# Optimization experiments

Hardware: AMD Instinct MI355X
Metric: run time of the kernel (lower is better)

## Reference

```python
import jax, jax.numpy as jnp
import numpy as np

# Matcher thresholds from detectron2 RPN defaults
IOU_LO, IOU_HI = 0.3, 0.7            # anchor_matcher
OBJ_LO, OBJ_HI = 0.1, 0.3            # objectness_anchor_matcher (lower thresholds)
EPS = 1e-12


def _pairwise_iou(gt, anc):
    # gt: [G,4], anc: [A,4] (x1,y1,x2,y2) -> [G,A]
    area_g = (gt[:, 2] - gt[:, 0]) * (gt[:, 3] - gt[:, 1])
    area_a = (anc[:, 2] - anc[:, 0]) * (anc[:, 3] - anc[:, 1])
    lt = jnp.maximum(gt[:, None, :2], anc[None, :, :2])
    rb = jnp.minimum(gt[:, None, 2:], anc[None, :, 2:])
    wh = jnp.clip(rb - lt, 0.0)
    inter = wh[..., 0] * wh[..., 1]
    union = area_g[:, None] + area_a[None, :] - inter
    return jnp.where(inter > 0, inter / union, 0.0)


def _match(iou, lo, hi):
    # detectron2 Matcher with labels [0,-1,1] and allow_low_quality_matches=True
    vals = iou.max(axis=0)                      # [A]
    idxs = jnp.argmax(iou, axis=0)              # [A]
    labels = jnp.where(vals >= hi, 1, jnp.where(vals >= lo, -1, 0)).astype(jnp.int32)
    highest_per_gt = iou.max(axis=1)            # [G]
    low_quality = (iou == highest_per_gt[:, None]).any(axis=0)  # [A]
    labels = jnp.where(low_quality, 1, labels)
    return idxs, labels


def _get_deltas_linear(anc, tgt):
    # Box2BoxTransformLinear(normalize_by_size=True).get_deltas
    cx = 0.5 * (anc[:, 0] + anc[:, 2])
    cy = 0.5 * (anc[:, 1] + anc[:, 3])
    w = anc[:, 2] - anc[:, 0]
    h = anc[:, 3] - anc[:, 1]
    # order (l, t, r, b)
    deltas = jnp.stack([cx - tgt[:, 0], cy - tgt[:, 1], tgt[:, 2] - cx, tgt[:, 3] - cy], axis=-1)
    return deltas / jnp.stack([w, h, w, h], axis=-1)


def _label_one_image(gt_i, anchors):
    iou = _pairwise_iou(gt_i, anchors)                     # [G,A]
    m_idx, gt_labels = _match(iou, IOU_LO, IOU_HI)
    o_idx, obj_labels = _match(iou, OBJ_LO, OBJ_HI)
    matched_gt_boxes = gt_i[m_idx]                         # [A,4]
    # deltas reordered [:, [0,2,1,3]] -> (left, right, top, bottom)
    d = _get_deltas_linear(anchors, gt_i[o_idx])[:, jnp.array([0, 2, 1, 3])]
    in_box = (d >= 0).all(axis=-1)
    d = jnp.where(in_box[:, None], d, 0.0)
    lr, tb = d[:, 0:2], d[:, 2:4]
    prod = (lr.min(-1) / (lr.max(-1) + EPS)) * (tb.min(-1) / (tb.max(-1) + EPS))
    centerness = jnp.where(prod > 0, jnp.sqrt(jnp.where(prod > 0, prod, 1.0)), 0.0)
    centerness = jnp.where(obj_labels == 0, 0.0, centerness)
    return gt_labels, matched_gt_boxes, obj_labels, centerness


def setup_inputs() -> dict:
    key = jax.random.key(0)
    k1, k2, k3, k4 = jax.random.split(key, 4)
    A, B, G = 200000, 8, 32
    img_wh = jnp.array([1333.0, 800.0], dtype=jnp.float32)
    # anchors: random centers, sizes in [8, 264]
    a_ctr = jax.random.uniform(k1, (A, 2), dtype=jnp.float32) * img_wh
    a_wh = jax.random.uniform(k2, (A, 2), dtype=jnp.float32) * 256.0 + 8.0
    anchors = jnp.concatenate([a_ctr - 0.5 * a_wh, a_ctr + 0.5 * a_wh], axis=-1)
    # gt boxes: [B,G,4], sizes in [16, 416]
    g_ctr = jax.random.uniform(k3, (B, G, 2), dtype=jnp.float32) * img_wh
    g_wh = jax.random.uniform(k4, (B, G, 2), dtype=jnp.float32) * 400.0 + 16.0
    gt_boxes = jnp.concatenate([g_ctr - 0.5 * g_wh, g_ctr + 0.5 * g_wh], axis=-1)
    return {"gt_boxes": gt_boxes, "anchors": anchors}


def reference(gt_boxes, anchors):
    # gt_boxes: [B,G,4]; anchors: [A,4]
    gt_labels, matched_gt_boxes, obj_labels, centerness = jax.vmap(
        lambda g: _label_one_image(g, anchors)
    )(gt_boxes)
    return gt_labels, matched_gt_boxes, obj_labels, centerness
```

## Files before the change

kernel.cpp:

```cpp
#include <hip/hip_runtime.h>

#define G 32
#define APT 4
#define CHUNK (256 * APT)

__device__ __forceinline__ float iou_pre(float sum_area,
                                         float g0, float g1, float g2, float g3,
                                         float a0, float a1, float a2, float a3) {
#pragma clang fp contract(off)
    float ltx = fmaxf(g0, a0), lty = fmaxf(g1, a1);
    float rbx = fminf(g2, a2), rby = fminf(g3, a3);
    float wx = fmaxf(rbx - ltx, 0.0f), wy = fmaxf(rby - lty, 0.0f);
    float inter = wx * wy;
    float uni = sum_area - inter;
    return inter * __builtin_amdgcn_rcpf(uni);
}

__device__ __forceinline__ float centerness_fn(float4 an, float4 tb) {
#pragma clang fp contract(off)
    float cx = 0.5f * (an.x + an.z), cy = 0.5f * (an.y + an.w);
    float w = an.z - an.x, h = an.w - an.y;
    float d0 = (cx - tb.x) / w;
    float d1 = (tb.z - cx) / w;
    float d2 = (cy - tb.y) / h;
    float d3 = (tb.w - cy) / h;
    bool inb = (d0 >= 0.0f) && (d1 >= 0.0f) && (d2 >= 0.0f) && (d3 >= 0.0f);
    if (!inb) { d0 = d1 = d2 = d3 = 0.0f; }
    float prod = (fminf(d0, d1) / (fmaxf(d0, d1) + 1e-12f)) *
                 (fminf(d2, d3) / (fmaxf(d2, d3) + 1e-12f));
    return prod > 0.0f ? sqrtf(prod) : 0.0f;
}

__global__ __launch_bounds__(256) void k1_main(const float* __restrict__ gt,
                                               const float* __restrict__ anchors,
                                               float* __restrict__ out,
                                               float* __restrict__ blockmax,
                                               int A, int B) {
#pragma clang fp contract(off)
    __shared__ float4 s_gt[G];
    __shared__ float s_red[G * 4];
    const int c = blockIdx.x, b = blockIdx.y, t = threadIdx.x;
    if (t < G) s_gt[t] = ((const float4*)gt)[b * G + t];

    const float4* __restrict__ gt4 = (const float4*)gt;

    float4 an[APT];
    float aa[APT], best[APT];
    int bidx[APT];
    bool valid[APT];
    const int abase = c * CHUNK + t;
#pragma unroll
    for (int k = 0; k < APT; ++k) {
        int a = abase + k * 256;
        valid[k] = (a < A);
        int ac = valid[k] ? a : (A - 1);
        an[k] = ((const float4*)anchors)[ac];
        aa[k] = (an[k].z - an[k].x) * (an[k].w - an[k].y);
        best[k] = -1.0f;
        bidx[k] = 0;
    }

    const int lane = t & 63, wid = t >> 6;

#pragma unroll 8
    for (int g = 0; g < G; ++g) {
        const float4 gb = gt4[b * G + g];
        const float ag = (gb.z - gb.x) * (gb.w - gb.y);
        float v[APT];
#pragma unroll
        for (int k = 0; k < APT; ++k) {
            v[k] = iou_pre(ag + aa[k], gb.x, gb.y, gb.z, gb.w,
                           an[k].x, an[k].y, an[k].z, an[k].w);
            if (v[k] > best[k]) { best[k] = v[k]; bidx[k] = g; }
        }
        float lm = fmaxf(fmaxf(v[0], v[1]), fmaxf(v[2], v[3]));
#pragma unroll
        for (int off = 32; off > 0; off >>= 1) lm = fmaxf(lm, __shfl_down(lm, off, 64));
        if (lane == 0) s_red[g * 4 + wid] = lm;
    }
    __syncthreads();
    if (t < G) {
        float v = fmaxf(fmaxf(s_red[t * 4 + 0], s_red[t * 4 + 1]),
                        fmaxf(s_red[t * 4 + 2], s_red[t * 4 + 3]));
        blockmax[(c * B + b) * G + t] = v;
    }

    const size_t BA = (size_t)B * (size_t)A;
    const size_t bA = (size_t)b * (size_t)A;
#pragma unroll
    for (int k = 0; k < APT; ++k) {
        if (!valid[k]) continue;
        const size_t o = bA + (size_t)(abase + k * 256);
        int gl = (best[k] >= 0.7f) ? 1 : ((best[k] >= 0.3f) ? -1 : 0);
        int ol = (best[k] >= 0.3f) ? 1 : ((best[k] >= 0.1f) ? -1 : 0);
        const float4 tb = s_gt[bidx[k]];
        float cen = centerness_fn(an[k], tb);
        if (ol == 0) cen = 0.0f;
        out[o] = (float)gl;
        ((float4*)(out + BA))[o] = tb;
        out[5 * BA + o] = (float)ol;
        out[6 * BA + o] = cen;
    }
}

__global__ void k2_reduce(const float* __restrict__ blockmax,
                          float* __restrict__ hi, int C, int BG) {
    const int bg = blockIdx.x, t = threadIdx.x;
    float v = 0.0f;
    for (int c = t; c < C; c += 64) v = fmaxf(v, blockmax[c * BG + bg]);
#pragma unroll
    for (int off = 32; off > 0; off >>= 1) v = fmaxf(v, __shfl_down(v, off, 64));
    if (t == 0) hi[bg] = v;
}

__global__ __launch_bounds__(256) void k3_patch(const float* __restrict__ gt,
                                                const float* __restrict__ anchors,
                                                const float* __restrict__ blockmax,
                                                const float* __restrict__ hi,
                                                float* __restrict__ out,
                                                int A, int B) {
#pragma clang fp contract(off)
    __shared__ float4 s_gt[G];
    __shared__ float s_hi[G];
    __shared__ unsigned s_mask;
    const int c = blockIdx.x, b = blockIdx.y, t = threadIdx.x;
    bool fl = false;
    if (t < G) {
        float h = hi[b * G + t];
        s_hi[t] = h;
        s_gt[t] = ((const float4*)gt)[b * G + t];
        fl = (blockmax[(c * B + b) * G + t] == h);
    }
    unsigned long long m = __ballot(fl);
    if (t == 0) s_mask = (unsigned)(m & 0xffffffffull);
    __syncthreads();
    const unsigned mask0 = s_mask;
    if (mask0 == 0) return;

    const size_t BA = (size_t)B * (size_t)A;
    const size_t bA = (size_t)b * (size_t)A;
    const int abase = c * CHUNK + t;

#pragma unroll
    for (int k = 0; k < APT; ++k) {
        const int a = abase + k * 256;
        if (a >= A) continue;
        const float4 an = ((const float4*)anchors)[a];
        const float aa = (an.z - an.x) * (an.w - an.y);
        bool lq = false;
        unsigned mask = mask0;
        while (mask) {
            const int g = __ffs(mask) - 1;
            mask &= mask - 1;
            const float4 gb = s_gt[g];
            const float ag = (gb.z - gb.x) * (gb.w - gb.y);
            const float v = iou_pre(ag + aa, gb.x, gb.y, gb.z, gb.w,
                                    an.x, an.y, an.z, an.w);
            lq |= (v == s_hi[g]);
        }
        if (lq) {
            const size_t o = bA + (size_t)a;
            const float4 tb = ((const float4*)(out + BA))[o];
            const float cen = centerness_fn(an, tb);
            out[o] = 1.0f;
            out[5 * BA + o] = 1.0f;
            out[6 * BA + o] = cen;
        }
    }
}

extern "C" void kernel_launch(void* const* d_in, const int* in_sizes, int n_in,
                              void* d_out, int out_size, void* d_ws, size_t ws_size,
                              hipStream_t stream) {
    const float* gt = (const float*)d_in[0];
    const float* anchors = (const float*)d_in[1];
    float* out = (float*)d_out;

    const int B = in_sizes[0] / (G * 4);
    const int A = in_sizes[1] / 4;
    const int C = (A + CHUNK - 1) / CHUNK;
    const int BG = B * G;

    float* hi = (float*)d_ws;
    float* blockmax = (float*)((char*)d_ws + 1024);

    k1_main<<<dim3(C, B), 256, 0, stream>>>(gt, anchors, out, blockmax, A, B);
    k2_reduce<<<BG, 64, 0, stream>>>(blockmax, hi, C, BG);
    k3_patch<<<dim3(C, B), 256, 0, stream>>>(gt, anchors, blockmax, hi, out, A, B);
}
```

Before: 119.8 us.

## Replace per-GT wave shuffle reductions with recursive-halving transpose reduction

Instead of doing a full 6-step shuffle max reduction for each of the 32 GT boxes, each thread keeps 32 per-GT maxima in registers. A recursive-halving butterfly exchange then leaves each lane holding the reduced max for one (bit-reversed) GT index. This cuts shuffle count from 32*6 to about 31+1 per wave. The cost is 32 extra live registers, a fully unrolled GT loop, and a bit-reversed output index that must be correct.

```diff
diff --git a/kernel.cpp b/kernel.cpp
--- a/kernel.cpp
+++ b/kernel.cpp
@@ -31,6 +31,10 @@
     return prod > 0.0f ? sqrtf(prod) : 0.0f;
 }
 
+__device__ __forceinline__ int rev5(int t) {
+    return ((t & 1) << 4) | ((t & 2) << 2) | (t & 4) | ((t & 8) >> 2) | ((t & 16) >> 4);
+}
+
 __global__ __launch_bounds__(256) void k1_main(const float* __restrict__ gt,
                                                const float* __restrict__ anchors,
                                                float* __restrict__ out,
@@ -38,7 +42,7 @@
                                                int A, int B) {
 #pragma clang fp contract(off)
     __shared__ float4 s_gt[G];
-    __shared__ float s_red[G * 4];
+    __shared__ float s_red[4 * 32];
     const int c = blockIdx.x, b = blockIdx.y, t = threadIdx.x;
     if (t < G) s_gt[t] = ((const float4*)gt)[b * G + t];
 
@@ -60,9 +64,9 @@
         bidx[k] = 0;
     }
 
-    const int lane = t & 63, wid = t >> 6;
-
-#pragma unroll 8
+    float lm[G];
+
+#pragma unroll
     for (int g = 0; g < G; ++g) {
         const float4 gb = gt4[b * G + g];
         const float ag = (gb.z - gb.x) * (gb.w - gb.y);
@@ -73,16 +77,31 @@
                            an[k].x, an[k].y, an[k].z, an[k].w);
             if (v[k] > best[k]) { best[k] = v[k]; bidx[k] = g; }
         }
-        float lm = fmaxf(fmaxf(v[0], v[1]), fmaxf(v[2], v[3]));
-#pragma unroll
-        for (int off = 32; off > 0; off >>= 1) lm = fmaxf(lm, __shfl_down(lm, off, 64));
-        if (lane == 0) s_red[g * 4 + wid] = lm;
+        lm[g] = fmaxf(fmaxf(v[0], v[1]), fmaxf(v[2], v[3]));
+    }
+
+    {
+        const int lane = t & 63, wid = t >> 6;
+#pragma unroll
+        for (int bit = 0; bit < 5; ++bit) {
+            const int s = 1 << bit;
+            const int L2 = 16 >> bit;
+            const bool hi = (lane & s) != 0;
+#pragma unroll
+            for (int i = 0; i < L2; ++i) {
+                float send = hi ? lm[i] : lm[L2 + i];
+                float keep = hi ? lm[L2 + i] : lm[i];
+                lm[i] = fmaxf(keep, __shfl_xor(send, s, 64));
+            }
+        }
+        float v = fmaxf(lm[0], __shfl_xor(lm[0], 32, 64));
+        if (lane < 32) s_red[wid * 32 + lane] = v;
     }
     __syncthreads();
-    if (t < G) {
-        float v = fmaxf(fmaxf(s_red[t * 4 + 0], s_red[t * 4 + 1]),
-                        fmaxf(s_red[t * 4 + 2], s_red[t * 4 + 3]));
-        blockmax[(c * B + b) * G + t] = v;
+    if (t < 32) {
+        float m = fmaxf(fmaxf(s_red[t], s_red[32 + t]),
+                        fmaxf(s_red[64 + t], s_red[96 + t]));
+        blockmax[(c * B + b) * G + rev5(t)] = m;
     }
 
     const size_t BA = (size_t)B * (size_t)A;
```

Result: slower. 157.8 us (+31.7%).
